# Kernel tuning notes

Hardware: AMD Instinct MI355X
Metric: run time of the kernel (lower is better)

## Reference

```python
import jax, jax.numpy as jnp
import numpy as np

B, D_IN, D_H = 8192, 2048, 2048


def _glorot(key, shape, fan_in):
    bound = 1.0 / np.sqrt(fan_in)
    return jax.random.uniform(key, shape, jnp.float32, -bound, bound)


def setup_inputs() -> dict:
    key = jax.random.key(0)
    ks = jax.random.split(key, 16)
    inp = {
        'x': jax.random.normal(ks[0], (B, D_IN), jnp.float32),
        'h': jax.random.normal(ks[1], (B, D_H), jnp.float32),
        'c': jax.random.normal(ks[2], (B, D_H), jnp.float32),
    }
    # Linear weights stored torch-style: W [out, in], y = x @ W.T + b
    names = ['Wix', 'Wmx', 'Wox']
    for i, n in enumerate(names):
        inp[n] = _glorot(ks[3 + i], (D_H, D_IN), D_IN)
        inp['b' + n[1:]] = _glorot(ks[6 + i], (D_H,), D_IN)
    names_h = ['Wih', 'Wmh', 'Woh']
    for i, n in enumerate(names_h):
        inp[n] = _glorot(ks[9 + i], (D_H, D_H), D_H)
        inp['b' + n[1:]] = _glorot(ks[12 + i], (D_H,), D_H)
    return inp


def reference(x, h, c, Wix, bix, Wmx, bmx, Wox, box, Wih, bih, Wmh, bmh, Woh, boh):
    # Fuse the 3 distinct x-GEMMs and 3 h-GEMMs into two concatenated GEMMs.
    Wx = jnp.concatenate([Wix, Wmx, Wox], axis=0)   # [3H, D_IN]
    Wh = jnp.concatenate([Wih, Wmh, Woh], axis=0)   # [3H, D_H]
    bx = jnp.concatenate([bix, bmx, box])
    bh = jnp.concatenate([bih, bmh, boh])
    g = x @ Wx.T + bx + h @ Wh.T + bh               # [B, 3H]
    gi, gm, go = jnp.split(g, 3, axis=-1)
    input_state = jax.nn.sigmoid(gi)
    # Faithful to source: memory gate pre-activation used for BOTH
    # the sigmoid "forget" gate and the tanh candidate (forgot_gate_* unused).
    forgot_state = jax.nn.sigmoid(gm)
    memory_state = jnp.tanh(gm)
    output_state = jax.nn.sigmoid(go)
    c_new = forgot_state * c + input_state * memory_state
    h_new = output_state * jnp.tanh(c_new)
    return (h_new, c_new)
```

## Files before the change

### kernel.cpp

```cpp
#include <hip/hip_runtime.h>

#define DEV __device__ __forceinline__

typedef __bf16 bf16x8 __attribute__((ext_vector_type(8)));
typedef float f32x4 __attribute__((ext_vector_type(4)));
typedef unsigned short ushort8 __attribute__((ext_vector_type(8)));

constexpr int BATCH = 8192;
constexpr int HD    = 2048;
constexpr size_t NX   = (size_t)BATCH * HD;
constexpr size_t NW   = (size_t)HD * HD;
constexpr size_t NTOT = 2 * NX + 6 * NW;

DEV unsigned short f2bf(float f) {
    unsigned int v = __builtin_bit_cast(unsigned int, f);
    unsigned int r = (v + 0x7FFFu + ((v >> 16) & 1u)) >> 16;
    return (unsigned short)r;
}
DEV float sigm(float v)  { return 1.0f / (1.0f + __expf(-v)); }
DEV float tanh_(float v) {
    float z = fminf(fmaxf(v, -15.0f), 15.0f);
    float e = __expf(2.0f * z);
    return (e - 1.0f) / (e + 1.0f);
}

DEV void gl16(const unsigned short* g, unsigned short* lds_uniform_base) {
    __builtin_amdgcn_global_load_lds(
        (const __attribute__((address_space(1))) unsigned int*)g,
        (__attribute__((address_space(3))) unsigned int*)lds_uniform_base,
        16, 0, 0);
}

__global__ __launch_bounds__(256) void cvt_all(
    const float* __restrict__ x,  const float* __restrict__ h,
    const float* __restrict__ w0, const float* __restrict__ w1,
    const float* __restrict__ w2, const float* __restrict__ w3,
    const float* __restrict__ w4, const float* __restrict__ w5,
    unsigned short* __restrict__ dst)
{
    const size_t base = (size_t)blockIdx.x * 2048;
    const float* src; size_t rel;
    if      (base <  NX)          { src = x;  rel = base; }
    else if (base < 2*NX)         { src = h;  rel = base - NX; }
    else if (base < 2*NX +   NW)  { src = w0; rel = base - 2*NX; }
    else if (base < 2*NX + 2*NW)  { src = w1; rel = base - (2*NX +   NW); }
    else if (base < 2*NX + 3*NW)  { src = w2; rel = base - (2*NX + 2*NW); }
    else if (base < 2*NX + 4*NW)  { src = w3; rel = base - (2*NX + 3*NW); }
    else if (base < 2*NX + 5*NW)  { src = w4; rel = base - (2*NX + 4*NW); }
    else                          { src = w5; rel = base - (2*NX + 5*NW); }
    const float* s = src + rel + threadIdx.x * 8;
    f32x4 u0 = *reinterpret_cast<const f32x4*>(s);
    f32x4 u1 = *reinterpret_cast<const f32x4*>(s + 4);
    ushort8 v;
#pragma unroll
    for (int j = 0; j < 4; ++j) { v[j] = f2bf(u0[j]); v[4 + j] = f2bf(u1[j]); }
    *reinterpret_cast<ushort8*>(dst + base + threadIdx.x * 8) = v;
}

__global__ __launch_bounds__(256, 2) void lstm_fast(
    const unsigned short* __restrict__ xb, const unsigned short* __restrict__ hb,
    const unsigned short* __restrict__ W0x, const unsigned short* __restrict__ W1x,
    const unsigned short* __restrict__ W2x, const unsigned short* __restrict__ W0h,
    const unsigned short* __restrict__ W1h, const unsigned short* __restrict__ W2h,
    const float* __restrict__ c,
    const float* __restrict__ bix, const float* __restrict__ bih,
    const float* __restrict__ bmx, const float* __restrict__ bmh,
    const float* __restrict__ box_, const float* __restrict__ boh,
    float* __restrict__ hout, float* __restrict__ cout)
{
    __shared__ unsigned short As [2][128 * 32];
    __shared__ unsigned short B0s[2][128 * 32];
    __shared__ unsigned short B1s[2][128 * 32];
    __shared__ unsigned short B2s[2][128 * 32];

    const int tid  = threadIdx.x;
    const int lane = tid & 63;
    const int wave = tid >> 6;

    const int n0 = blockIdx.x * 128;
    const int m0 = blockIdx.y * 128;

    const int arow = lane >> 2;
    const int acol = (lane & 3) * 8;

    const int mOff = (wave >> 1) * 64;
    const int nOff = (wave & 1) * 64;
    const int q    = lane >> 4;
    const int ml   = lane & 15;

    const int r0 = wave * 32, r1 = wave * 32 + 16;

    const size_t aoff0 = (size_t)(m0 + r0 + arow) * HD + acol;
    const size_t aoff1 = (size_t)(m0 + r1 + arow) * HD + acol;
    const size_t boff0 = (size_t)(n0 + r0 + arow) * HD + acol;
    const size_t boff1 = (size_t)(n0 + r1 + arow) * HD + acol;

    f32x4 a0[4][4] = {};
    f32x4 a1[4][4] = {};
    f32x4 a2[4][4] = {};

    auto stage = [&](int kt, int buf) {
        const int k0 = kt * 32;
        const unsigned short *Asrc, *W0, *W1, *W2;
        int kk;
        if (k0 < HD) { Asrc = xb; W0 = W0x; W1 = W1x; W2 = W2x; kk = k0; }
        else         { Asrc = hb; W0 = W0h; W1 = W1h; W2 = W2h; kk = k0 - HD; }
        gl16(Asrc + aoff0 + kk, &As [buf][r0 * 32]);
        gl16(Asrc + aoff1 + kk, &As [buf][r1 * 32]);
        gl16(W0   + boff0 + kk, &B0s[buf][r0 * 32]);
        gl16(W0   + boff1 + kk, &B0s[buf][r1 * 32]);
        gl16(W1   + boff0 + kk, &B1s[buf][r0 * 32]);
        gl16(W1   + boff1 + kk, &B1s[buf][r1 * 32]);
        gl16(W2   + boff0 + kk, &B2s[buf][r0 * 32]);
        gl16(W2   + boff1 + kk, &B2s[buf][r1 * 32]);
    };

    auto compute = [&](int buf) {
        bf16x8 af[4];
#pragma unroll
        for (int t = 0; t < 4; ++t)
            af[t] = *reinterpret_cast<const bf16x8*>(&As[buf][(mOff + t * 16 + ml) * 32 + q * 8]);
        {
            bf16x8 bfr[4];
#pragma unroll
            for (int tn = 0; tn < 4; ++tn)
                bfr[tn] = *reinterpret_cast<const bf16x8*>(&B0s[buf][(nOff + tn * 16 + ml) * 32 + q * 8]);
#pragma unroll
            for (int tm = 0; tm < 4; ++tm)
#pragma unroll
                for (int tn = 0; tn < 4; ++tn)
                    a0[tm][tn] = __builtin_amdgcn_mfma_f32_16x16x32_bf16(af[tm], bfr[tn], a0[tm][tn], 0, 0, 0);
        }
        {
            bf16x8 bfr[4];
#pragma unroll
            for (int tn = 0; tn < 4; ++tn)
                bfr[tn] = *reinterpret_cast<const bf16x8*>(&B1s[buf][(nOff + tn * 16 + ml) * 32 + q * 8]);
#pragma unroll
            for (int tm = 0; tm < 4; ++tm)
#pragma unroll
                for (int tn = 0; tn < 4; ++tn)
                    a1[tm][tn] = __builtin_amdgcn_mfma_f32_16x16x32_bf16(af[tm], bfr[tn], a1[tm][tn], 0, 0, 0);
        }
        {
            bf16x8 bfr[4];
#pragma unroll
            for (int tn = 0; tn < 4; ++tn)
                bfr[tn] = *reinterpret_cast<const bf16x8*>(&B2s[buf][(nOff + tn * 16 + ml) * 32 + q * 8]);
#pragma unroll
            for (int tm = 0; tm < 4; ++tm)
#pragma unroll
                for (int tn = 0; tn < 4; ++tn)
                    a2[tm][tn] = __builtin_amdgcn_mfma_f32_16x16x32_bf16(af[tm], bfr[tn], a2[tm][tn], 0, 0, 0);
        }
    };

    stage(0, 0);
    asm volatile("s_waitcnt vmcnt(0)" ::: "memory");
    __syncthreads();

    int cur = 0;
    for (int kt = 0; kt < 127; ++kt) {
        stage(kt + 1, cur ^ 1);
        compute(cur);
        asm volatile("s_waitcnt vmcnt(0)" ::: "memory");
        __syncthreads();
        cur ^= 1;
    }
    compute(cur);

#pragma unroll
    for (int tn = 0; tn < 4; ++tn) {
        const int col = n0 + nOff + tn * 16 + ml;
        const float Bi = bix[col] + bih[col];
        const float Bm = bmx[col] + bmh[col];
        const float Bo = box_[col] + boh[col];
#pragma unroll
        for (int tm = 0; tm < 4; ++tm) {
            const int rb = m0 + mOff + tm * 16 + q * 4;
#pragma unroll
            for (int r = 0; r < 4; ++r) {
                const size_t b = rb + r;
                const float cold = c[b * HD + col];
                const float gi = a0[tm][tn][r] + Bi;
                const float gm = a1[tm][tn][r] + Bm;
                const float go = a2[tm][tn][r] + Bo;
                const float i_s = sigm(gi);
                const float f_s = sigm(gm);
                const float m_s = tanh_(gm);
                const float o_s = sigm(go);
                const float cn  = f_s * cold + i_s * m_s;
                const float hn  = o_s * tanh_(cn);
                hout[b * HD + col] = hn;
                cout[b * HD + col] = cn;
            }
        }
    }
}

DEV void stage64f(unsigned short* lds, const float* src, size_t row_base, int kk, int tid) {
    const int r  = tid >> 2;
    const int cc = (tid & 3) * 8;
    const float* s = src + (row_base + r) * (size_t)HD + kk + cc;
    f32x4 u0 = *(const f32x4*)s;
    f32x4 u1 = *(const f32x4*)(s + 4);
    ushort8 v;
#pragma unroll
    for (int j = 0; j < 4; ++j) { v[j] = f2bf(u0[j]); v[4 + j] = f2bf(u1[j]); }
    *reinterpret_cast<ushort8*>(&lds[r * 32 + cc]) = v;
}

__global__ __launch_bounds__(256, 2) void lstm_slow(
    const float* __restrict__ x,   const float* __restrict__ h,
    const float* __restrict__ c,
    const float* __restrict__ Wix, const float* __restrict__ bix,
    const float* __restrict__ Wmx, const float* __restrict__ bmx,
    const float* __restrict__ Wox, const float* __restrict__ box_,
    const float* __restrict__ Wih, const float* __restrict__ bih,
    const float* __restrict__ Wmh, const float* __restrict__ bmh,
    const float* __restrict__ Woh, const float* __restrict__ boh,
    float* __restrict__ hout, float* __restrict__ cout)
{
    __shared__ unsigned short As[64 * 32];
    __shared__ unsigned short B0s[128 * 32];
    __shared__ unsigned short B1s[128 * 32];
    __shared__ unsigned short B2s[128 * 32];

    const int tid  = threadIdx.x;
    const int lane = tid & 63;
    const int wave = tid >> 6;
    const int n0 = blockIdx.x * 128;
    const int m0 = blockIdx.y * 64;
    const int mOff = (wave >> 1) * 32;
    const int nOff = (wave & 1) * 64;
    const int q    = lane >> 4;
    const int ml   = lane & 15;

    f32x4 a0[2][4] = {}; f32x4 a1[2][4] = {}; f32x4 a2[2][4] = {};

    auto kstep = [&](const float* Asrc, const float* W0, const float* W1,
                     const float* W2, int kk) {
        stage64f(As, Asrc, m0, kk, tid & 255);
        stage64f(B0s,           W0, n0,      kk, tid);
        stage64f(B0s + 64 * 32, W0, n0 + 64, kk, tid);
        stage64f(B1s,           W1, n0,      kk, tid);
        stage64f(B1s + 64 * 32, W1, n0 + 64, kk, tid);
        stage64f(B2s,           W2, n0,      kk, tid);
        stage64f(B2s + 64 * 32, W2, n0 + 64, kk, tid);
        __syncthreads();
        bf16x8 af[2], bfr[4];
        af[0] = *reinterpret_cast<const bf16x8*>(&As[(mOff      + ml) * 32 + q * 8]);
        af[1] = *reinterpret_cast<const bf16x8*>(&As[(mOff + 16 + ml) * 32 + q * 8]);
#pragma unroll
        for (int tn = 0; tn < 4; ++tn)
            bfr[tn] = *reinterpret_cast<const bf16x8*>(&B0s[(nOff + tn * 16 + ml) * 32 + q * 8]);
#pragma unroll
        for (int tm = 0; tm < 2; ++tm)
#pragma unroll
            for (int tn = 0; tn < 4; ++tn)
                a0[tm][tn] = __builtin_amdgcn_mfma_f32_16x16x32_bf16(af[tm], bfr[tn], a0[tm][tn], 0, 0, 0);
#pragma unroll
        for (int tn = 0; tn < 4; ++tn)
            bfr[tn] = *reinterpret_cast<const bf16x8*>(&B1s[(nOff + tn * 16 + ml) * 32 + q * 8]);
#pragma unroll
        for (int tm = 0; tm < 2; ++tm)
#pragma unroll
            for (int tn = 0; tn < 4; ++tn)
                a1[tm][tn] = __builtin_amdgcn_mfma_f32_16x16x32_bf16(af[tm], bfr[tn], a1[tm][tn], 0, 0, 0);
#pragma unroll
        for (int tn = 0; tn < 4; ++tn)
            bfr[tn] = *reinterpret_cast<const bf16x8*>(&B2s[(nOff + tn * 16 + ml) * 32 + q * 8]);
#pragma unroll
        for (int tm = 0; tm < 2; ++tm)
#pragma unroll
            for (int tn = 0; tn < 4; ++tn)
                a2[tm][tn] = __builtin_amdgcn_mfma_f32_16x16x32_bf16(af[tm], bfr[tn], a2[tm][tn], 0, 0, 0);
        __syncthreads();
    };

    for (int kt = 0; kt < 64; ++kt) kstep(x, Wix, Wmx, Wox, kt * 32);
    for (int kt = 0; kt < 64; ++kt) kstep(h, Wih, Wmh, Woh, kt * 32);

#pragma unroll
    for (int tn = 0; tn < 4; ++tn) {
        const int col = n0 + nOff + tn * 16 + ml;
        const float Bi = bix[col] + bih[col];
        const float Bm = bmx[col] + bmh[col];
        const float Bo = box_[col] + boh[col];
#pragma unroll
        for (int tm = 0; tm < 2; ++tm) {
            const int rb = m0 + mOff + tm * 16 + q * 4;
#pragma unroll
            for (int r = 0; r < 4; ++r) {
                const size_t b = rb + r;
                const float cold = c[b * HD + col];
                const float gi = a0[tm][tn][r] + Bi;
                const float gm = a1[tm][tn][r] + Bm;
                const float go = a2[tm][tn][r] + Bo;
                const float cn = sigm(gm) * cold + sigm(gi) * tanh_(gm);
                const float hn = sigm(go) * tanh_(cn);
                hout[b * HD + col] = hn;
                cout[b * HD + col] = cn;
            }
        }
    }
}

extern "C" void kernel_launch(void* const* d_in, const int* in_sizes, int n_in,
                              void* d_out, int out_size, void* d_ws, size_t ws_size,
                              hipStream_t stream) {
    const float* x   = (const float*)d_in[0];
    const float* h   = (const float*)d_in[1];
    const float* c   = (const float*)d_in[2];
    const float* Wix = (const float*)d_in[3];  const float* bix = (const float*)d_in[4];
    const float* Wmx = (const float*)d_in[5];  const float* bmx = (const float*)d_in[6];
    const float* Wox = (const float*)d_in[7];  const float* box_= (const float*)d_in[8];
    const float* Wih = (const float*)d_in[9];  const float* bih = (const float*)d_in[10];
    const float* Wmh = (const float*)d_in[11]; const float* bmh = (const float*)d_in[12];
    const float* Woh = (const float*)d_in[13]; const float* boh = (const float*)d_in[14];

    float* hout = (float*)d_out;
    float* cout = hout + NX;

    if (ws_size >= NTOT * sizeof(unsigned short)) {
        unsigned short* ws = (unsigned short*)d_ws;
        cvt_all<<<dim3((unsigned)(NTOT / 2048)), dim3(256), 0, stream>>>(
            x, h, Wix, Wmx, Wox, Wih, Wmh, Woh, ws);

        const unsigned short* xb  = ws;
        const unsigned short* hb  = ws + NX;
        const unsigned short* W0x = ws + 2 * NX;
        const unsigned short* W1x = ws + 2 * NX + NW;
        const unsigned short* W2x = ws + 2 * NX + 2 * NW;
        const unsigned short* W0h = ws + 2 * NX + 3 * NW;
        const unsigned short* W1h = ws + 2 * NX + 4 * NW;
        const unsigned short* W2h = ws + 2 * NX + 5 * NW;

        lstm_fast<<<dim3(HD / 128, BATCH / 128), dim3(256), 0, stream>>>(
            xb, hb, W0x, W1x, W2x, W0h, W1h, W2h,
            c, bix, bih, bmx, bmh, box_, boh, hout, cout);
    } else {
        lstm_slow<<<dim3(HD / 128, BATCH / 64), dim3(256), 0, stream>>>(
            x, h, c, Wix, bix, Wmx, bmx, Wox, box_,
            Wih, bih, Wmh, bmh, Woh, boh, hout, cout);
    }
}
```

Measured before the change: 848.6 us.

## Restructure K-loop into two-stage prefetch with partial vmcnt waits

The main GEMM loop now issues loads for two K-tiles ahead and waits only until the older tile's loads have landed (vmcnt(8)), instead of draining all outstanding loads each iteration. The loop is unrolled by two with fixed buffer indices, and uses raw s_barrier plus sched_barrier in place of __syncthreads. The aim is to keep global loads in flight across compute so memory latency is hidden. Correctness depends on the vmcnt count matching the number of loads per stage and on the barriers around buffer reuse being placed correctly.

Measured after the change: 793.8 us. 6.5% less time.

```diff
diff --git a/kernel.cpp b/kernel.cpp
--- a/kernel.cpp
+++ b/kernel.cpp
@@ -156,18 +156,32 @@
     };
 
     stage(0, 0);
+    stage(1, 1);
+    asm volatile("s_waitcnt vmcnt(8)" ::: "memory");
+    __builtin_amdgcn_s_barrier();
+    __builtin_amdgcn_sched_barrier(0);
+
+#pragma unroll 1
+    for (int kt = 0; kt < 126; kt += 2) {
+        compute(0);
+        __builtin_amdgcn_s_barrier();
+        stage(kt + 2, 0);
+        asm volatile("s_waitcnt vmcnt(8)" ::: "memory");
+        __builtin_amdgcn_s_barrier();
+        __builtin_amdgcn_sched_barrier(0);
+        compute(1);
+        __builtin_amdgcn_s_barrier();
+        stage(kt + 3, 1);
+        asm volatile("s_waitcnt vmcnt(8)" ::: "memory");
+        __builtin_amdgcn_s_barrier();
+        __builtin_amdgcn_sched_barrier(0);
+    }
+    compute(0);
+    __builtin_amdgcn_s_barrier();
     asm volatile("s_waitcnt vmcnt(0)" ::: "memory");
-    __syncthreads();
-
-    int cur = 0;
-    for (int kt = 0; kt < 127; ++kt) {
-        stage(kt + 1, cur ^ 1);
-        compute(cur);
-        asm volatile("s_waitcnt vmcnt(0)" ::: "memory");
-        __syncthreads();
-        cur ^= 1;
-    }
-    compute(cur);
+    __builtin_amdgcn_s_barrier();
+    __builtin_amdgcn_sched_barrier(0);
+    compute(1);
 
 #pragma unroll
     for (int tn = 0; tn < 4; ++tn) {
```
